# Performance work log

Measured on AMD Instinct MI355X. Metric: run time of the kernel, lower is better.

Reference implementation:

```python
import jax, jax.numpy as jnp
import numpy as np

BS, CLS, C, H, W = 8, 4, 256, 128, 128
L, TK = 19, 256
MH, MW = 64, 64


def setup_inputs() -> dict:
    key = jax.random.key(0)
    ks = jax.random.split(key, 7)
    return {
        "mask_t": jax.random.uniform(ks[0], (BS, CLS, 1, MH, MW), dtype=jnp.float32),
        "fea_t": jax.random.normal(ks[1], (BS, C, H, W), dtype=jnp.float32),
        "token_s": jax.random.normal(ks[2], (BS, L, TK), dtype=jnp.float32),
        "W1": jax.random.normal(ks[3], (TK, C), dtype=jnp.float32) / np.sqrt(C),
        "W2": jax.random.normal(ks[4], (TK, TK), dtype=jnp.float32) / np.sqrt(TK),
        "W3": jax.random.normal(ks[5], (C, TK), dtype=jnp.float32) / np.sqrt(TK),
        "b3": jnp.zeros((C,), dtype=jnp.float32),
    }


def reference(mask_t, fea_t, token_s, W1, W2, W3, b3):
    bs, c, h, w = fea_t.shape
    cls = mask_t.shape[1]
    mh, mw = mask_t.shape[-2], mask_t.shape[-1]
    # F.interpolate nearest: out index i -> in index floor(i * in/out)
    ri = (jnp.arange(h) * mh) // h
    ci = (jnp.arange(w) * mw) // w
    m = mask_t.reshape(bs * cls, 1, mh, mw)[:, :, ri][:, :, :, ci]  # [bs*cls,1,h,w]
    # replicate torch's fea_t.repeat(cls,1,1,1) ordering (copy-major: index c*bs+b)
    # then the product is re-viewed batch-major (b*cls+c): fea index = (b*cls+cl) % bs
    idx = jnp.arange(bs * cls) % bs
    fea_c = (fea_t[idx] * m).reshape(bs, cls, c, h, w).mean(axis=1)  # [bs,c,h,w]
    q = fea_c.reshape(bs, c, h * w).transpose(0, 2, 1)  # [bs, HW, C]
    # forward_cell
    x_q = jnp.einsum('bnc,tc->bnt', q, W1)            # [bs,HW,TK]
    t_q = jnp.einsum('blc,tc->blt', token_s, W2)      # [bs,L,TK]
    a = jnp.einsum('bnt,blt->bnl', x_q, t_q)          # [bs,HW,L]
    a_soft = jax.nn.softmax(a / jnp.sqrt(jnp.float32(c)), axis=2)
    # sparse nonzero round-trip == zero out positions where logits are exactly 0
    a_soft = jnp.where(a != 0, a_soft, jnp.float32(0))
    t3 = jnp.einsum('blt,ot->blo', token_s, W3) + b3  # [bs,L,out]
    out = jnp.einsum('bnl,blo->bno', a_soft, t3)      # [bs,HW,out]
    out = out.transpose(0, 2, 1).reshape(bs, c, h, w)
    return out + fea_t
```

## Files before the change

kernel.cpp:

```cpp
#include <hip/hip_runtime.h>
#include <math.h>

#define BS   8
#define CLS  4
#define CCH  256
#define HH   128
#define WW   128
#define HWSZ (HH * WW)
#define LL   19
#define TKK  256
#define MHH  64
#define MWW  64

__global__ __launch_bounds__(256) void k_tr(
    const float* __restrict__ W2, const float* __restrict__ W3,
    float* __restrict__ W2T, float* __restrict__ W3T) {
  __shared__ float tile[64][65];
  const int blk = blockIdx.x;
  const int m   = blk >> 4;
  const int q   = blk & 15;
  const int tr  = (q >> 2) * 64;
  const int tc  = (q & 3) * 64;
  const float* src = (m == 0) ? W2 : W3;
  float*       dst = (m == 0) ? W2T : W3T;
  const int t  = threadIdx.x;
  const int c  = t & 63;
  const int r0 = t >> 6;
#pragma unroll
  for (int rp = 0; rp < 64; rp += 4)
    tile[rp + r0][c] = src[(size_t)(tr + rp + r0) * TKK + tc + c];
  __syncthreads();
#pragma unroll
  for (int rp = 0; rp < 64; rp += 4)
    dst[(size_t)(tc + rp + r0) * TKK + tr + c] = tile[c][rp + r0];
}

__global__ __launch_bounds__(256) void k_prep_tr(
    const float* __restrict__ token, const float* __restrict__ W1,
    const float* __restrict__ W2T, const float* __restrict__ W3T,
    const float* __restrict__ b3, float* __restrict__ u,
    float* __restrict__ t3t) {
  __shared__ float tok_s[TKK];
  __shared__ float tq_s[TKK];
  const int bl = blockIdx.x;
  const int b  = bl / LL;
  const int l  = bl - b * LL;
  const int t  = threadIdx.x;
  tok_s[t] = token[(size_t)bl * TKK + t];
  __syncthreads();
  float a2a = 0.f, a2b = 0.f, a3a = 0.f, a3b = 0.f;
#pragma unroll 8
  for (int k = 0; k < TKK; k += 2) {
    const float w2a = W2T[(size_t)(k + 0) * TKK + t];
    const float w2b = W2T[(size_t)(k + 1) * TKK + t];
    const float w3a = W3T[(size_t)(k + 0) * TKK + t];
    const float w3b = W3T[(size_t)(k + 1) * TKK + t];
    a2a += w2a * tok_s[k + 0];
    a2b += w2b * tok_s[k + 1];
    a3a += w3a * tok_s[k + 0];
    a3b += w3b * tok_s[k + 1];
  }
  tq_s[t] = a2a + a2b;
  t3t[((size_t)b * CCH + t) * 20 + l] = a3a + a3b + b3[t];
  __syncthreads();
  float s0 = 0.f, s1 = 0.f, s2 = 0.f, s3 = 0.f;
#pragma unroll 8
  for (int k = 0; k < TKK; k += 4) {
    s0 += W1[(size_t)(k + 0) * CCH + t] * tq_s[k + 0];
    s1 += W1[(size_t)(k + 1) * CCH + t] * tq_s[k + 1];
    s2 += W1[(size_t)(k + 2) * CCH + t] * tq_s[k + 2];
    s3 += W1[(size_t)(k + 3) * CCH + t] * tq_s[k + 3];
  }
  u[(size_t)bl * CCH + t] = (s0 + s1 + s2 + s3) * (1.0f / 64.0f);
}

__global__ __launch_bounds__(256) void k_prep_leg(
    const float* __restrict__ token, const float* __restrict__ W1,
    const float* __restrict__ W2, const float* __restrict__ W3,
    const float* __restrict__ b3, float* __restrict__ u,
    float* __restrict__ t3t) {
  __shared__ float tok_s[TKK];
  __shared__ float tq_s[TKK];
  const int bl = blockIdx.x;
  const int b  = bl / LL;
  const int l  = bl - b * LL;
  const int t  = threadIdx.x;
  tok_s[t] = token[(size_t)bl * TKK + t];
  __syncthreads();
  const float4* w2r = (const float4*)(W2 + (size_t)t * TKK);
  const float4* w3r = (const float4*)(W3 + (size_t)t * TKK);
  float a2 = 0.f, a3 = 0.f;
#pragma unroll 8
  for (int i = 0; i < TKK / 4; ++i) {
    float4 x = w2r[i];
    float4 y = w3r[i];
    const float* ts = &tok_s[4 * i];
    a2 += x.x * ts[0] + x.y * ts[1] + x.z * ts[2] + x.w * ts[3];
    a3 += y.x * ts[0] + y.y * ts[1] + y.z * ts[2] + y.w * ts[3];
  }
  tq_s[t] = a2;
  t3t[((size_t)b * CCH + t) * 20 + l] = a3 + b3[t];
  __syncthreads();
  float s0 = 0.f, s1 = 0.f, s2 = 0.f, s3 = 0.f;
#pragma unroll 4
  for (int k = 0; k < TKK; k += 4) {
    s0 += W1[(k + 0) * CCH + t] * tq_s[k + 0];
    s1 += W1[(k + 1) * CCH + t] * tq_s[k + 1];
    s2 += W1[(k + 2) * CCH + t] * tq_s[k + 2];
    s3 += W1[(k + 3) * CCH + t] * tq_s[k + 3];
  }
  u[(size_t)bl * CCH + t] = (s0 + s1 + s2 + s3) * (1.0f / 64.0f);
}

__global__ __launch_bounds__(512, 4) void k_main(
    const float* __restrict__ mask, const float* __restrict__ fea,
    const float* __restrict__ u, const float* __restrict__ t3t,
    float* __restrict__ out) {
  __shared__ float4 sh_buf4[(CCH * 20) / 4];
  __shared__ float acc_s[LL][128];
  float* sh_buf = (float*)sh_buf4;

  const int blk  = blockIdx.x;
  const int b    = blk & 7;
  const int tile = blk >> 3;
  const int n0   = tile * WW;
  const int t    = threadIdx.x;
  const int lane = t & 63;
  const int wv   = t >> 6;

  for (int k = t; k < LL * CCH; k += 512)
    sh_buf[k] = u[(size_t)b * LL * CCH + k];
  for (int k = t; k < LL * 128; k += 512) ((float*)acc_s)[k] = 0.f;

  const int hrow = tile >> 1;
  const size_t mbase = (((size_t)(b * CLS)) * MHH + hrow) * MWW + lane;
  const float m0 = mask[mbase + (size_t)0 * MHH * MWW];
  const float m1 = mask[mbase + (size_t)1 * MHH * MWW];
  const float m2 = mask[mbase + (size_t)2 * MHH * MWW];
  const float m3 = mask[mbase + (size_t)3 * MHH * MWW];

  __syncthreads();

  const int f0 = (b & 1) * 4;
  const float* fb0 = fea + (size_t)(f0 + 0) * CCH * HWSZ + n0;
  const float* fb1 = fea + (size_t)(f0 + 1) * CCH * HWSZ + n0;
  const float* fb2 = fea + (size_t)(f0 + 2) * CCH * HWSZ + n0;
  const float* fb3 = fea + (size_t)(f0 + 3) * CCH * HWSZ + n0;

  float facc[LL][2];
#pragma unroll
  for (int l = 0; l < LL; ++l) { facc[l][0] = 0.f; facc[l][1] = 0.f; }

  const int c0 = wv * 32;
#pragma unroll 2
  for (int cc = 0; cc < 32; cc += 4) {
    float2 q[4];
#pragma unroll
    for (int j = 0; j < 4; ++j) {
      const size_t coff = (size_t)(c0 + cc + j) * HWSZ;
      const float2 v0 = ((const float2*)(fb0 + coff))[lane];
      const float2 v1 = ((const float2*)(fb1 + coff))[lane];
      const float2 v2 = ((const float2*)(fb2 + coff))[lane];
      const float2 v3 = ((const float2*)(fb3 + coff))[lane];
      q[j].x = v0.x * m0 + v1.x * m1 + v2.x * m2 + v3.x * m3;
      q[j].y = v0.y * m0 + v1.y * m1 + v2.y * m2 + v3.y * m3;
    }
#pragma unroll
    for (int l = 0; l < LL; ++l) {
      const float4 uu = *(const float4*)&sh_buf[l * CCH + c0 + cc];
      facc[l][0] += q[0].x * uu.x + q[1].x * uu.y + q[2].x * uu.z + q[3].x * uu.w;
      facc[l][1] += q[0].y * uu.x + q[1].y * uu.y + q[2].y * uu.z + q[3].y * uu.w;
    }
  }

#pragma unroll
  for (int l = 0; l < LL; ++l) {
    atomicAdd(&acc_s[l][2 * lane + 0], facc[l][0]);
    atomicAdd(&acc_s[l][2 * lane + 1], facc[l][1]);
  }
  __syncthreads();

  {
    const float* t3b = t3t + (size_t)b * CCH * 20;
    for (int k = t; k < CCH * 20; k += 512) sh_buf[k] = t3b[k];
  }
  if (t < 128) {
    float a[LL];
    float mx = -INFINITY;
#pragma unroll
    for (int l = 0; l < LL; ++l) { a[l] = acc_s[l][t]; mx = fmaxf(mx, a[l]); }
    float e[LL];
    float sum = 0.f;
#pragma unroll
    for (int l = 0; l < LL; ++l) { e[l] = __expf(a[l] - mx); sum += e[l]; }
    const float inv = 1.0f / sum;
#pragma unroll
    for (int l = 0; l < LL; ++l)
      acc_s[l][t] = (a[l] != 0.f) ? e[l] * inv : 0.f;
  }
  __syncthreads();

  float2 p[LL];
#pragma unroll
  for (int l = 0; l < LL; ++l) p[l] = *(const float2*)&acc_s[l][2 * lane];

  const int wvu = __builtin_amdgcn_readfirstlane(wv);
  const int ob  = wvu * 32;
  for (int i0 = 0; i0 < 32; i0 += 4) {
    float2 r[4];
#pragma unroll
    for (int j = 0; j < 4; ++j) {
      const size_t off = ((size_t)b * CCH + ob + i0 + j) * HWSZ + n0;
      r[j] = ((const float2*)(fea + off))[lane];
    }
#pragma unroll
    for (int j = 0; j < 4; ++j) {
      const int o = ob + i0 + j;
      const float4* tv = (const float4*)&sh_buf[o * 20];
      const float4 A = tv[0], B = tv[1], C = tv[2], D = tv[3], E = tv[4];
      const float sx =
          p[0].x  * A.x + p[1].x  * A.y + p[2].x  * A.z + p[3].x  * A.w +
          p[4].x  * B.x + p[5].x  * B.y + p[6].x  * B.z + p[7].x  * B.w +
          p[8].x  * C.x + p[9].x  * C.y + p[10].x * C.z + p[11].x * C.w +
          p[12].x * D.x + p[13].x * D.y + p[14].x * D.z + p[15].x * D.w +
          p[16].x * E.x + p[17].x * E.y + p[18].x * E.z;
      const float sy =
          p[0].y  * A.x + p[1].y  * A.y + p[2].y  * A.z + p[3].y  * A.w +
          p[4].y  * B.x + p[5].y  * B.y + p[6].y  * B.z + p[7].y  * B.w +
          p[8].y  * C.x + p[9].y  * C.y + p[10].y * C.z + p[11].y * C.w +
          p[12].y * D.x + p[13].y * D.y + p[14].y * D.z + p[15].y * D.w +
          p[16].y * E.x + p[17].y * E.y + p[18].y * E.z;
      const size_t off = ((size_t)b * CCH + o) * HWSZ + n0;
      float2 res;
      res.x = sx + r[j].x;
      res.y = sy + r[j].y;
      ((float2*)(out + off))[lane] = res;
    }
  }
}

extern "C" void kernel_launch(void* const* d_in, const int* in_sizes, int n_in,
                              void* d_out, int out_size, void* d_ws, size_t ws_size,
                              hipStream_t stream) {
  (void)in_sizes; (void)n_in; (void)out_size;
  const float* mask  = (const float*)d_in[0];
  const float* fea   = (const float*)d_in[1];
  const float* token = (const float*)d_in[2];
  const float* W1    = (const float*)d_in[3];
  const float* W2    = (const float*)d_in[4];
  const float* W3    = (const float*)d_in[5];
  const float* b3    = (const float*)d_in[6];
  float* out = (float*)d_out;

  float* u   = (float*)d_ws;
  float* t3t = u + BS * LL * CCH;
  float* W2T = t3t + BS * CCH * 20;
  float* W3T = W2T + TKK * TKK;
  const size_t ws_need =
      (size_t)(BS * LL * CCH + BS * CCH * 20 + 2 * TKK * TKK) * sizeof(float);

  if (ws_size >= ws_need) {
    k_tr<<<32, 256, 0, stream>>>(W2, W3, W2T, W3T);
    k_prep_tr<<<BS * LL, 256, 0, stream>>>(token, W1, W2T, W3T, b3, u, t3t);
  } else {
    k_prep_leg<<<BS * LL, 256, 0, stream>>>(token, W1, W2, W3, b3, u, t3t);
  }
  k_main<<<(HWSZ / WW) * BS, 512, 0, stream>>>(mask, fea, u, t3t, out);
}
```

Measured before the change: 419.8 us.

## Halve main-kernel block size and double-buffer fea loads in projection loop

The main kernel drops from 512 to 256 threads per block, so each wave now covers 64 channels instead of 32. The projection loop gains explicit register double-buffering: the next 4-channel group of fea loads is issued while the current group is consumed, to hide global memory latency. The t3 staging into shared memory is removed, and the output stage reads t3t rows straight from global memory with uniform per-wave addresses. In exchange, register pressure rises from the two load buffers, occupancy may drop, and each thread runs a longer serial loop.

New measurement: 354.6 us. 1.18x faster.

```diff
diff --git a/kernel.cpp b/kernel.cpp
--- a/kernel.cpp
+++ b/kernel.cpp
@@ -112,13 +112,45 @@
   u[(size_t)bl * CCH + t] = (s0 + s1 + s2 + s3) * (1.0f / 64.0f);
 }
 
-__global__ __launch_bounds__(512, 4) void k_main(
+#define LOADC(buf, k)                                                        \
+  {                                                                          \
+    const size_t coff_ = (size_t)(c0 + (k) * 4) * HWSZ;                      \
+    _Pragma("unroll")                                                        \
+    for (int j = 0; j < 4; ++j) {                                            \
+      const size_t co_ = coff_ + (size_t)j * HWSZ;                           \
+      buf[j][0] = ((const float2*)(fb0 + co_))[lane];                        \
+      buf[j][1] = ((const float2*)(fb1 + co_))[lane];                        \
+      buf[j][2] = ((const float2*)(fb2 + co_))[lane];                        \
+      buf[j][3] = ((const float2*)(fb3 + co_))[lane];                        \
+    }                                                                        \
+  }
+
+#define CONSC(buf, k)                                                        \
+  {                                                                          \
+    float2 q_[4];                                                            \
+    _Pragma("unroll")                                                        \
+    for (int j = 0; j < 4; ++j) {                                            \
+      q_[j].x = buf[j][0].x * m0 + buf[j][1].x * m1 +                        \
+                buf[j][2].x * m2 + buf[j][3].x * m3;                         \
+      q_[j].y = buf[j][0].y * m0 + buf[j][1].y * m1 +                        \
+                buf[j][2].y * m2 + buf[j][3].y * m3;                         \
+    }                                                                        \
+    _Pragma("unroll")                                                        \
+    for (int l = 0; l < LL; ++l) {                                           \
+      const float4 uu = *(const float4*)&u_s[l][c0 + (k) * 4];               \
+      facc[l][0] += q_[0].x * uu.x + q_[1].x * uu.y +                        \
+                    q_[2].x * uu.z + q_[3].x * uu.w;                         \
+      facc[l][1] += q_[0].y * uu.x + q_[1].y * uu.y +                        \
+                    q_[2].y * uu.z + q_[3].y * uu.w;                         \
+    }                                                                        \
+  }
+
+__global__ __launch_bounds__(256, 2) void k_main(
     const float* __restrict__ mask, const float* __restrict__ fea,
     const float* __restrict__ u, const float* __restrict__ t3t,
     float* __restrict__ out) {
-  __shared__ float4 sh_buf4[(CCH * 20) / 4];
+  __shared__ float u_s[LL][CCH];
   __shared__ float acc_s[LL][128];
-  float* sh_buf = (float*)sh_buf4;
 
   const int blk  = blockIdx.x;
   const int b    = blk & 7;
@@ -128,16 +160,15 @@
   const int lane = t & 63;
   const int wv   = t >> 6;
 
-  for (int k = t; k < LL * CCH; k += 512)
-    sh_buf[k] = u[(size_t)b * LL * CCH + k];
-  for (int k = t; k < LL * 128; k += 512) ((float*)acc_s)[k] = 0.f;
+#pragma unroll
+  for (int l = 0; l < LL; ++l) u_s[l][t] = u[((size_t)b * LL + l) * CCH + t];
+  for (int k = t; k < LL * 128; k += 256) ((float*)acc_s)[k] = 0.f;
 
   const int hrow = tile >> 1;
-  const size_t mbase = (((size_t)(b * CLS)) * MHH + hrow) * MWW + lane;
-  const float m0 = mask[mbase + (size_t)0 * MHH * MWW];
-  const float m1 = mask[mbase + (size_t)1 * MHH * MWW];
-  const float m2 = mask[mbase + (size_t)2 * MHH * MWW];
-  const float m3 = mask[mbase + (size_t)3 * MHH * MWW];
+  const float m0 = mask[(((size_t)(b * CLS + 0)) * MHH + hrow) * MWW + lane];
+  const float m1 = mask[(((size_t)(b * CLS + 1)) * MHH + hrow) * MWW + lane];
+  const float m2 = mask[(((size_t)(b * CLS + 2)) * MHH + hrow) * MWW + lane];
+  const float m3 = mask[(((size_t)(b * CLS + 3)) * MHH + hrow) * MWW + lane];
 
   __syncthreads();
 
@@ -151,25 +182,17 @@
 #pragma unroll
   for (int l = 0; l < LL; ++l) { facc[l][0] = 0.f; facc[l][1] = 0.f; }
 
-  const int c0 = wv * 32;
-#pragma unroll 2
-  for (int cc = 0; cc < 32; cc += 4) {
-    float2 q[4];
-#pragma unroll
-    for (int j = 0; j < 4; ++j) {
-      const size_t coff = (size_t)(c0 + cc + j) * HWSZ;
-      const float2 v0 = ((const float2*)(fb0 + coff))[lane];
-      const float2 v1 = ((const float2*)(fb1 + coff))[lane];
-      const float2 v2 = ((const float2*)(fb2 + coff))[lane];
-      const float2 v3 = ((const float2*)(fb3 + coff))[lane];
-      q[j].x = v0.x * m0 + v1.x * m1 + v2.x * m2 + v3.x * m3;
-      q[j].y = v0.y * m0 + v1.y * m1 + v2.y * m2 + v3.y * m3;
-    }
-#pragma unroll
-    for (int l = 0; l < LL; ++l) {
-      const float4 uu = *(const float4*)&sh_buf[l * CCH + c0 + cc];
-      facc[l][0] += q[0].x * uu.x + q[1].x * uu.y + q[2].x * uu.z + q[3].x * uu.w;
-      facc[l][1] += q[0].y * uu.x + q[1].y * uu.y + q[2].y * uu.z + q[3].y * uu.w;
+  const int c0 = wv * 64;
+
+  {
+    float2 A[4][4], B[4][4];
+    LOADC(A, 0);
+#pragma unroll
+    for (int k = 0; k < 16; k += 2) {
+      LOADC(B, k + 1);
+      CONSC(A, k);
+      if (k + 2 < 16) LOADC(A, k + 2);
+      CONSC(B, k + 1);
     }
   }
 
@@ -180,10 +203,6 @@
   }
   __syncthreads();
 
-  {
-    const float* t3b = t3t + (size_t)b * CCH * 20;
-    for (int k = t; k < CCH * 20; k += 512) sh_buf[k] = t3b[k];
-  }
   if (t < 128) {
     float a[LL];
     float mx = -INFINITY;
@@ -205,37 +224,24 @@
   for (int l = 0; l < LL; ++l) p[l] = *(const float2*)&acc_s[l][2 * lane];
 
   const int wvu = __builtin_amdgcn_readfirstlane(wv);
-  const int ob  = wvu * 32;
-  for (int i0 = 0; i0 < 32; i0 += 4) {
-    float2 r[4];
-#pragma unroll
-    for (int j = 0; j < 4; ++j) {
-      const size_t off = ((size_t)b * CCH + ob + i0 + j) * HWSZ + n0;
-      r[j] = ((const float2*)(fea + off))[lane];
+  const int ob  = wvu * 64;
+#pragma unroll 4
+  for (int i = 0; i < 64; ++i) {
+    const int o = ob + i;
+    const float* tr = t3t + ((size_t)b * CCH + o) * 20;
+    float sx = 0.f, sy = 0.f;
+#pragma unroll
+    for (int l = 0; l < LL; ++l) {
+      const float tv = tr[l];
+      sx += p[l].x * tv;
+      sy += p[l].y * tv;
     }
-#pragma unroll
-    for (int j = 0; j < 4; ++j) {
-      const int o = ob + i0 + j;
-      const float4* tv = (const float4*)&sh_buf[o * 20];
-      const float4 A = tv[0], B = tv[1], C = tv[2], D = tv[3], E = tv[4];
-      const float sx =
-          p[0].x  * A.x + p[1].x  * A.y + p[2].x  * A.z + p[3].x  * A.w +
-          p[4].x  * B.x + p[5].x  * B.y + p[6].x  * B.z + p[7].x  * B.w +
-          p[8].x  * C.x + p[9].x  * C.y + p[10].x * C.z + p[11].x * C.w +
-          p[12].x * D.x + p[13].x * D.y + p[14].x * D.z + p[15].x * D.w +
-          p[16].x * E.x + p[17].x * E.y + p[18].x * E.z;
-      const float sy =
-          p[0].y  * A.x + p[1].y  * A.y + p[2].y  * A.z + p[3].y  * A.w +
-          p[4].y  * B.x + p[5].y  * B.y + p[6].y  * B.z + p[7].y  * B.w +
-          p[8].y  * C.x + p[9].y  * C.y + p[10].y * C.z + p[11].y * C.w +
-          p[12].y * D.x + p[13].y * D.y + p[14].y * D.z + p[15].y * D.w +
-          p[16].y * E.x + p[17].y * E.y + p[18].y * E.z;
-      const size_t off = ((size_t)b * CCH + o) * HWSZ + n0;
-      float2 res;
-      res.x = sx + r[j].x;
-      res.y = sy + r[j].y;
-      ((float2*)(out + off))[lane] = res;
-    }
+    const size_t off = ((size_t)b * CCH + o) * HWSZ + n0;
+    const float2 r = ((const float2*)(fea + off))[lane];
+    float2 res;
+    res.x = sx + r.x;
+    res.y = sy + r.y;
+    ((float2*)(out + off))[lane] = res;
   }
 }
 
@@ -265,5 +271,5 @@
   } else {
     k_prep_leg<<<BS * LL, 256, 0, stream>>>(token, W1, W2, W3, b3, u, t3t);
   }
-  k_main<<<(HWSZ / WW) * BS, 512, 0, stream>>>(mask, fea, u, t3t, out);
-}
+  k_main<<<(HWSZ / WW) * BS, 256, 0, stream>>>(mask, fea, u, t3t, out);
+}
```
